# Optimization experiments

Hardware: AMD Instinct MI355X
Metric: run time of the kernel (lower is better)

The kernel has to match this reference:

```python
import jax, jax.numpy as jnp
import numpy as np

BITS = 4
GROUP = 128
M, K, N = 16, 4096, 11008


def setup_inputs() -> dict:
    key = jax.random.key(0)
    k1, k2, k3 = jax.random.split(key, 3)
    A = jax.random.normal(k1, (M, K), dtype=jnp.float16)
    # packed 4-bit weights: 2 nibbles per byte, stored as int32 holding 0..255
    qweight = jax.random.randint(k2, (N, K * BITS // 8), 0, 256, dtype=jnp.int32)
    # small positive-ish scales like real GPTQ checkpoints
    scales = (jax.random.normal(k3, (N, K // GROUP)) * 0.01 + 0.02).astype(jnp.float16)
    zeros = jnp.zeros((N, K // GROUP), dtype=jnp.float16)
    bias = jnp.zeros((N,), dtype=jnp.float16)
    return {"A": A, "qweight": qweight, "scales": scales, "zeros": zeros, "bias": bias}


def _dequant(qweight, scales, zeros):
    # qweight: (N, K//2) packed; element idx -> byte idx//2, low nibble if idx even
    low = qweight & 0xF
    high = (qweight >> 4) & 0xF
    w_int = jnp.stack([low, high], axis=-1).reshape(qweight.shape[0], -1)  # (N, K)
    # per-group dequant with 'original' zeros: W = (q - z) * s
    s = jnp.repeat(scales, GROUP, axis=1)  # (N, K)
    z = jnp.repeat(zeros, GROUP, axis=1)   # (N, K)
    return (w_int.astype(jnp.float16) - z) * s


def reference(A, qweight, scales, zeros, bias):
    W = _dequant(qweight, scales, zeros)           # (N, K) fp16
    return jnp.matmul(A, W.T) + bias               # (M, N) fp16
```

## Files before the change

kernel.cpp:

```cpp
#include <hip/hip_runtime.h>

#define KK 4096
#define NN 11008
#define NGRP 32
#define KW 2048
#define WS_RS_OFF 131072
#define WS_SZ_OFF 139264

using short8  = __attribute__((ext_vector_type(8))) short;
using float4v = __attribute__((ext_vector_type(4))) float;

static __device__ __forceinline__ unsigned int pack_bf16(float lo, float hi) {
    unsigned int ul = __builtin_bit_cast(unsigned int, lo);
    unsigned int uh = __builtin_bit_cast(unsigned int, hi);
    ul = (ul + 0x7FFFu + ((ul >> 16) & 1u)) >> 16;
    uh = (uh + 0x7FFFu + ((uh >> 16) & 1u)) & 0xFFFF0000u;
    return ul | uh;
}
static __device__ __forceinline__ float bf16val(float f) {
    unsigned int u = __builtin_bit_cast(unsigned int, f);
    u = (u + 0x7FFFu + ((u >> 16) & 1u)) & 0xFFFF0000u;
    return __builtin_bit_cast(float, u);
}

__global__ __launch_bounds__(256) void prep_kernel(
    const float* __restrict__ A, const float* __restrict__ scales,
    const float* __restrict__ zeros, unsigned short* __restrict__ wsA,
    float* __restrict__ rowsum, float* __restrict__ SZ)
{
    const int b = blockIdx.x, t = threadIdx.x;
    if (b < 32) {
        const int tid = b * 256 + t;
        const int c = tid >> 6, l = tid & 63;
        const float* src = A + (size_t)(l & 15) * KK + c * 32 + (l >> 4) * 8;
        float4v x0 = *(const float4v*)src;
        float4v x1 = *(const float4v*)(src + 4);
        union { short8 s8; unsigned int u[4]; } p;
        p.u[0] = pack_bf16(x0[0], x0[1]);
        p.u[1] = pack_bf16(x0[2], x0[3]);
        p.u[2] = pack_bf16(x1[0], x1[1]);
        p.u[3] = pack_bf16(x1[2], x1[3]);
        *(short8*)(wsA + (size_t)tid * 8) = p.s8;
    } else if (b < 64) {
        const int sid = (b - 32) * 16 + (t >> 4);
        const int m = sid >> 5, g = sid & 31, j = t & 15;
        const float* p = A + (size_t)m * KK + g * 128 + j * 8;
        float4v x0 = *(const float4v*)p;
        float4v x1 = *(const float4v*)(p + 4);
        float sum = bf16val(x0[0]) + bf16val(x0[1]) + bf16val(x0[2]) + bf16val(x0[3])
                  + bf16val(x1[0]) + bf16val(x1[1]) + bf16val(x1[2]) + bf16val(x1[3]);
        sum += __shfl_xor(sum, 1, 16);
        sum += __shfl_xor(sum, 2, 16);
        sum += __shfl_xor(sum, 4, 16);
        sum += __shfl_xor(sum, 8, 16);
        if (j == 0) rowsum[sid] = sum;
    } else {
        const int e0 = (b - 64) * 1024 + t * 4;
        float4v s4 = *(const float4v*)(scales + e0);
        float4v z4 = *(const float4v*)(zeros + e0);
        float4v r;
        #pragma unroll
        for (int j = 0; j < 4; ++j) r[j] = s4[j] * (128.0f + z4[j]);
        *(float4v*)(SZ + e0) = r;
    }
}

__global__ __launch_bounds__(256) void init_out_kernel(
    const float* __restrict__ bias, const float* __restrict__ SZ,
    const float* __restrict__ rowsum, float* __restrict__ out)
{
    __shared__ float rs[16][32];
    const int t = threadIdx.x;
    rs[t >> 5][t & 31]       = rowsum[t];
    rs[(t >> 5) + 8][t & 31] = rowsum[t + 256];
    __syncthreads();
    const int n0 = blockIdx.x * 16;
    const int m = t >> 4, nn = t & 15, ng = n0 + nn;
    const float* szr = SZ + (size_t)ng * NGRP;
    float corr = 0.f;
    #pragma unroll
    for (int g = 0; g < 32; ++g)
        corr = __builtin_fmaf(szr[g], rs[m][g], corr);
    out[(size_t)m * NN + ng] = bias[ng] - corr;
}

__global__ __launch_bounds__(256) void qgemm_kernel(
    const int*            __restrict__ qweight,
    const float*          __restrict__ scales,
    const unsigned short* __restrict__ aperm,
    float*                __restrict__ out)
{
    const int nt = blockIdx.x >> 3, slice = blockIdx.x & 7;
    const int n0 = nt * 16;
    const int wid = threadIdx.x >> 6, lane = threadIdx.x & 63;
    const int nl = lane & 15, quad = lane >> 4;
    const int n = n0 + nl;
    const int g = slice * 4 + wid;

    const int* qrow = qweight + (size_t)n * KW + g * 64 + quad * 4;
    const unsigned short* ap = aperm + (size_t)g * 2048 + lane * 8;

    int4   w0 = *(const int4*)(qrow);
    int4   w1 = *(const int4*)(qrow + 16);
    int4   w2 = *(const int4*)(qrow + 32);
    int4   w3 = *(const int4*)(qrow + 48);
    short8 a0 = *(const short8*)(ap);
    short8 a1 = *(const short8*)(ap + 512);
    short8 a2 = *(const short8*)(ap + 1024);
    short8 a3 = *(const short8*)(ap + 1536);
    const float s = scales[n * NGRP + g];

    float4v acc = {0.f, 0.f, 0.f, 0.f};
    int4 wv[4] = {w0, w1, w2, w3};
    short8 av[4] = {a0, a1, a2, a3};
    #pragma unroll
    for (int t = 0; t < 4; ++t) {
        const unsigned int x0 = (unsigned int)wv[t].x, x1 = (unsigned int)wv[t].y;
        const unsigned int x2 = (unsigned int)wv[t].z, x3 = (unsigned int)wv[t].w;
        union { short8 s8; unsigned int u[4]; } bf;
        bf.u[0] = (x0 & 0xFu) | ((x0 << 12) & 0x000F0000u) | 0x43004300u;
        bf.u[1] = (x1 & 0xFu) | ((x1 << 12) & 0x000F0000u) | 0x43004300u;
        bf.u[2] = (x2 & 0xFu) | ((x2 << 12) & 0x000F0000u) | 0x43004300u;
        bf.u[3] = (x3 & 0xFu) | ((x3 << 12) & 0x000F0000u) | 0x43004300u;
        acc = __builtin_amdgcn_mfma_f32_16x16x32_bf16(av[t], bf.s8, acc, 0, 0, 0);
    }

    __shared__ float red[4][16][16];
    #pragma unroll
    for (int r = 0; r < 4; ++r)
        red[wid][quad * 4 + r][nl] = s * acc[r];
    __syncthreads();

    const int t = threadIdx.x;
    const int m = t >> 4, nn = t & 15;
    float val = red[0][m][nn] + red[1][m][nn] + red[2][m][nn] + red[3][m][nn];
    atomicAdd(&out[(size_t)m * NN + n0 + nn], val);
}

extern "C" void kernel_launch(void* const* d_in, const int* in_sizes, int n_in,
                              void* d_out, int out_size, void* d_ws, size_t ws_size,
                              hipStream_t stream) {
    const float* A       = (const float*)d_in[0];
    const int*   qweight = (const int*)d_in[1];
    const float* scales  = (const float*)d_in[2];
    const float* zeros   = (const float*)d_in[3];
    const float* bias    = (const float*)d_in[4];
    float*       out     = (float*)d_out;

    unsigned short* wsA = (unsigned short*)d_ws;
    float* rowsum       = (float*)((char*)d_ws + WS_RS_OFF);
    float* SZ           = (float*)((char*)d_ws + WS_SZ_OFF);

    prep_kernel<<<dim3(408), dim3(256), 0, stream>>>(A, scales, zeros, wsA, rowsum, SZ);
    init_out_kernel<<<dim3(688), dim3(256), 0, stream>>>(bias, SZ, rowsum, out);
    qgemm_kernel<<<dim3(5504), dim3(256), 0, stream>>>(qweight, scales, wsA, out);
}
```

Measured before the change: 144.3 us.

## Stage weight tiles through LDS with coalesced loads and larger K-slices per block

Each block now covers half of K for 16 output columns instead of one eighth. It first loads a 64KB weight tile with fully coalesced row-contiguous 16-byte loads into shared memory, then each wave reads its MFMA operands from LDS and applies per-group scales in registers. This replaces strided per-lane global reads of qweight and cuts the number of blocks and atomics by a factor of four. In exchange, the large LDS footprint limits occupancy, and there is a serial load-then-compute phase with no overlap.

Result: slower. 148.1 us (+2.6%).

```diff
diff --git a/kernel.cpp b/kernel.cpp
--- a/kernel.cpp
+++ b/kernel.cpp
@@ -84,56 +84,71 @@
     out[(size_t)m * NN + ng] = bias[ng] - corr;
 }
 
-__global__ __launch_bounds__(256) void qgemm_kernel(
+__global__ __launch_bounds__(256, 2) void qgemm_kernel(
     const int*            __restrict__ qweight,
     const float*          __restrict__ scales,
     const unsigned short* __restrict__ aperm,
     float*                __restrict__ out)
 {
-    const int nt = blockIdx.x >> 3, slice = blockIdx.x & 7;
+    __shared__ __align__(16) char tile[65536];
+
+    const int nt = blockIdx.x >> 1, kh = blockIdx.x & 1;
     const int n0 = nt * 16;
     const int wid = threadIdx.x >> 6, lane = threadIdx.x & 63;
     const int nl = lane & 15, quad = lane >> 4;
-    const int n = n0 + nl;
-    const int g = slice * 4 + wid;
 
-    const int* qrow = qweight + (size_t)n * KW + g * 64 + quad * 4;
-    const unsigned short* ap = aperm + (size_t)g * 2048 + lane * 8;
+    const char* gbase = (const char*)qweight + (size_t)n0 * 8192 + kh * 4096;
+    int4 stg[16];
+    #pragma unroll
+    for (int i = 0; i < 16; ++i) {
+        const int r = wid * 4 + (i >> 2), c = i & 3;
+        stg[i] = *(const int4*)(gbase + (size_t)r * 8192 + c * 1024 + (lane << 4));
+    }
+    #pragma unroll
+    for (int i = 0; i < 16; ++i) {
+        const int r = wid * 4 + (i >> 2), c = i & 3;
+        *(int4*)(tile + r * 4096 + c * 1024 + (lane << 4)) = stg[i];
+    }
+    __syncthreads();
 
-    int4   w0 = *(const int4*)(qrow);
-    int4   w1 = *(const int4*)(qrow + 16);
-    int4   w2 = *(const int4*)(qrow + 32);
-    int4   w3 = *(const int4*)(qrow + 48);
-    short8 a0 = *(const short8*)(ap);
-    short8 a1 = *(const short8*)(ap + 512);
-    short8 a2 = *(const short8*)(ap + 1024);
-    short8 a3 = *(const short8*)(ap + 1536);
-    const float s = scales[n * NGRP + g];
-
+    const float* srow = scales + (size_t)(n0 + nl) * NGRP + kh * 16 + wid * 4;
     float4v acc = {0.f, 0.f, 0.f, 0.f};
-    int4 wv[4] = {w0, w1, w2, w3};
-    short8 av[4] = {a0, a1, a2, a3};
     #pragma unroll
-    for (int t = 0; t < 4; ++t) {
-        const unsigned int x0 = (unsigned int)wv[t].x, x1 = (unsigned int)wv[t].y;
-        const unsigned int x2 = (unsigned int)wv[t].z, x3 = (unsigned int)wv[t].w;
-        union { short8 s8; unsigned int u[4]; } bf;
-        bf.u[0] = (x0 & 0xFu) | ((x0 << 12) & 0x000F0000u) | 0x43004300u;
-        bf.u[1] = (x1 & 0xFu) | ((x1 << 12) & 0x000F0000u) | 0x43004300u;
-        bf.u[2] = (x2 & 0xFu) | ((x2 << 12) & 0x000F0000u) | 0x43004300u;
-        bf.u[3] = (x3 & 0xFu) | ((x3 << 12) & 0x000F0000u) | 0x43004300u;
-        acc = __builtin_amdgcn_mfma_f32_16x16x32_bf16(av[t], bf.s8, acc, 0, 0, 0);
+    for (int gl = 0; gl < 4; ++gl) {
+        const int ch0 = wid * 16 + gl * 4;
+        float4v accg = {0.f, 0.f, 0.f, 0.f};
+        #pragma unroll
+        for (int t = 0; t < 4; ++t) {
+            const unsigned short* ap =
+                aperm + (size_t)(kh * 64 + ch0 + t) * 512 + lane * 8;
+            short8 a = *(const short8*)ap;
+            int4 wv = *(const int4*)(tile + nl * 4096 + (ch0 + t) * 64 + quad * 16);
+            const unsigned int x0 = (unsigned int)wv.x, x1 = (unsigned int)wv.y;
+            const unsigned int x2 = (unsigned int)wv.z, x3 = (unsigned int)wv.w;
+            union { short8 s8; unsigned int u[4]; } bf;
+            bf.u[0] = (x0 & 0xFu) | ((x0 << 12) & 0x000F0000u) | 0x43004300u;
+            bf.u[1] = (x1 & 0xFu) | ((x1 << 12) & 0x000F0000u) | 0x43004300u;
+            bf.u[2] = (x2 & 0xFu) | ((x2 << 12) & 0x000F0000u) | 0x43004300u;
+            bf.u[3] = (x3 & 0xFu) | ((x3 << 12) & 0x000F0000u) | 0x43004300u;
+            accg = __builtin_amdgcn_mfma_f32_16x16x32_bf16(a, bf.s8, accg, 0, 0, 0);
+        }
+        const float sg = srow[gl];
+        #pragma unroll
+        for (int r = 0; r < 4; ++r)
+            acc[r] = __builtin_fmaf(sg, accg[r], acc[r]);
     }
 
-    __shared__ float red[4][16][16];
+    __syncthreads();
+    float* red = (float*)tile;
     #pragma unroll
     for (int r = 0; r < 4; ++r)
-        red[wid][quad * 4 + r][nl] = s * acc[r];
+        red[wid * 256 + (quad * 4 + r) * 16 + nl] = acc[r];
     __syncthreads();
 
     const int t = threadIdx.x;
     const int m = t >> 4, nn = t & 15;
-    float val = red[0][m][nn] + red[1][m][nn] + red[2][m][nn] + red[3][m][nn];
+    float val = red[m * 16 + nn] + red[256 + m * 16 + nn]
+              + red[512 + m * 16 + nn] + red[768 + m * 16 + nn];
     atomicAdd(&out[(size_t)m * NN + n0 + nn], val);
 }
 
@@ -153,5 +168,5 @@
 
     prep_kernel<<<dim3(408), dim3(256), 0, stream>>>(A, scales, zeros, wsA, rowsum, SZ);
     init_out_kernel<<<dim3(688), dim3(256), 0, stream>>>(bias, SZ, rowsum, out);
-    qgemm_kernel<<<dim3(5504), dim3(256), 0, stream>>>(qweight, scales, wsA, out);
+    qgemm_kernel<<<dim3(1376), dim3(256), 0, stream>>>(qweight, scales, wsA, out);
 }
```

## Compact int32-per-byte weights into a packed byte buffer before the GEMM

Applied to the files above, without the earlier changes.

Adds a compaction stage to the prep kernel that reads the int32 qweight array and writes one byte per element into a workspace buffer. The layout is permuted so each GEMM lane gets its 16 bytes with a single 16-byte load instead of four. The GEMM then reads a quarter of the weight bytes. The catch is that the compaction runs on every call and must itself read the full 4-byte-per-element array and write the packed copy, so total memory traffic per call goes up rather than down.

Measured after the change: 156.3 us. +8.3%, slower.

```diff
diff --git a/kernel.cpp b/kernel.cpp
--- a/kernel.cpp
+++ b/kernel.cpp
@@ -3,9 +3,9 @@
 #define KK 4096
 #define NN 11008
 #define NGRP 32
-#define KW 2048
-#define WS_RS_OFF 131072
-#define WS_SZ_OFF 139264
+#define WS_RS_OFF  131072
+#define WS_SZ_OFF  139264
+#define WS_PK_OFF  2097152
 
 using short8  = __attribute__((ext_vector_type(8))) short;
 using float4v = __attribute__((ext_vector_type(4))) float;
@@ -23,14 +23,31 @@
     return __builtin_bit_cast(float, u);
 }
 
-__global__ __launch_bounds__(256) void prep_kernel(
-    const float* __restrict__ A, const float* __restrict__ scales,
-    const float* __restrict__ zeros, unsigned short* __restrict__ wsA,
-    float* __restrict__ rowsum, float* __restrict__ SZ)
+__global__ __launch_bounds__(256) void compact_prep_kernel(
+    const float* __restrict__ A, const int* __restrict__ qweight,
+    const float* __restrict__ scales, const float* __restrict__ zeros,
+    unsigned short* __restrict__ wsA, float* __restrict__ rowsum,
+    float* __restrict__ SZ, unsigned char* __restrict__ packed)
 {
     const int b = blockIdx.x, t = threadIdx.x;
-    if (b < 32) {
-        const int tid = b * 256 + t;
+    if (b < 5504) {
+        const int r  = t >> 7;
+        const int g  = (t >> 2) & 31;
+        const int tt = t & 3;
+        const size_t n = (size_t)b * 2 + r;
+        const int4* src = (const int4*)(qweight + n * 2048 + g * 64 + tt * 16);
+        unsigned char* dst = packed + n * 2048 + g * 64 + tt * 4;
+        #pragma unroll
+        for (int q = 0; q < 4; ++q) {
+            int4 v = src[q];
+            unsigned int d = ((unsigned int)v.x & 0xFFu)
+                           | (((unsigned int)v.y & 0xFFu) << 8)
+                           | (((unsigned int)v.z & 0xFFu) << 16)
+                           | (((unsigned int)v.w & 0xFFu) << 24);
+            *(unsigned int*)(dst + q * 16) = d;
+        }
+    } else if (b < 5536) {
+        const int tid = (b - 5504) * 256 + t;
         const int c = tid >> 6, l = tid & 63;
         const float* src = A + (size_t)(l & 15) * KK + c * 32 + (l >> 4) * 8;
         float4v x0 = *(const float4v*)src;
@@ -41,8 +58,8 @@
         p.u[2] = pack_bf16(x1[0], x1[1]);
         p.u[3] = pack_bf16(x1[2], x1[3]);
         *(short8*)(wsA + (size_t)tid * 8) = p.s8;
-    } else if (b < 64) {
-        const int sid = (b - 32) * 16 + (t >> 4);
+    } else if (b < 5568) {
+        const int sid = (b - 5536) * 16 + (t >> 4);
         const int m = sid >> 5, g = sid & 31, j = t & 15;
         const float* p = A + (size_t)m * KK + g * 128 + j * 8;
         float4v x0 = *(const float4v*)p;
@@ -55,7 +72,7 @@
         sum += __shfl_xor(sum, 8, 16);
         if (j == 0) rowsum[sid] = sum;
     } else {
-        const int e0 = (b - 64) * 1024 + t * 4;
+        const int e0 = (b - 5568) * 1024 + t * 4;
         float4v s4 = *(const float4v*)(scales + e0);
         float4v z4 = *(const float4v*)(zeros + e0);
         float4v r;
@@ -85,7 +102,7 @@
 }
 
 __global__ __launch_bounds__(256) void qgemm_kernel(
-    const int*            __restrict__ qweight,
+    const unsigned char*  __restrict__ packed,
     const float*          __restrict__ scales,
     const unsigned short* __restrict__ aperm,
     float*                __restrict__ out)
@@ -97,13 +114,10 @@
     const int n = n0 + nl;
     const int g = slice * 4 + wid;
 
-    const int* qrow = qweight + (size_t)n * KW + g * 64 + quad * 4;
+    const int4* wp = (const int4*)(packed + (size_t)n * 2048 + g * 64 + quad * 16);
     const unsigned short* ap = aperm + (size_t)g * 2048 + lane * 8;
 
-    int4   w0 = *(const int4*)(qrow);
-    int4   w1 = *(const int4*)(qrow + 16);
-    int4   w2 = *(const int4*)(qrow + 32);
-    int4   w3 = *(const int4*)(qrow + 48);
+    int4   wv = *wp;
     short8 a0 = *(const short8*)(ap);
     short8 a1 = *(const short8*)(ap + 512);
     short8 a2 = *(const short8*)(ap + 1024);
@@ -111,17 +125,18 @@
     const float s = scales[n * NGRP + g];
 
     float4v acc = {0.f, 0.f, 0.f, 0.f};
-    int4 wv[4] = {w0, w1, w2, w3};
+    const unsigned int dv[4] = {(unsigned int)wv.x, (unsigned int)wv.y,
+                                (unsigned int)wv.z, (unsigned int)wv.w};
     short8 av[4] = {a0, a1, a2, a3};
     #pragma unroll
     for (int t = 0; t < 4; ++t) {
-        const unsigned int x0 = (unsigned int)wv[t].x, x1 = (unsigned int)wv[t].y;
-        const unsigned int x2 = (unsigned int)wv[t].z, x3 = (unsigned int)wv[t].w;
+        const unsigned int d = dv[t];
+        const unsigned int c0 = d, c1 = d >> 8, c2 = d >> 16, c3 = d >> 24;
         union { short8 s8; unsigned int u[4]; } bf;
-        bf.u[0] = (x0 & 0xFu) | ((x0 << 12) & 0x000F0000u) | 0x43004300u;
-        bf.u[1] = (x1 & 0xFu) | ((x1 << 12) & 0x000F0000u) | 0x43004300u;
-        bf.u[2] = (x2 & 0xFu) | ((x2 << 12) & 0x000F0000u) | 0x43004300u;
-        bf.u[3] = (x3 & 0xFu) | ((x3 << 12) & 0x000F0000u) | 0x43004300u;
+        bf.u[0] = (c0 & 0xFu) | ((c0 << 12) & 0x000F0000u) | 0x43004300u;
+        bf.u[1] = (c1 & 0xFu) | ((c1 << 12) & 0x000F0000u) | 0x43004300u;
+        bf.u[2] = (c2 & 0xFu) | ((c2 << 12) & 0x000F0000u) | 0x43004300u;
+        bf.u[3] = (c3 & 0xFu) | ((c3 << 12) & 0x000F0000u) | 0x43004300u;
         acc = __builtin_amdgcn_mfma_f32_16x16x32_bf16(av[t], bf.s8, acc, 0, 0, 0);
     }
 
@@ -147,11 +162,13 @@
     const float* bias    = (const float*)d_in[4];
     float*       out     = (float*)d_out;
 
-    unsigned short* wsA = (unsigned short*)d_ws;
-    float* rowsum       = (float*)((char*)d_ws + WS_RS_OFF);
-    float* SZ           = (float*)((char*)d_ws + WS_SZ_OFF);
+    unsigned short* wsA   = (unsigned short*)d_ws;
+    float* rowsum         = (float*)((char*)d_ws + WS_RS_OFF);
+    float* SZ             = (float*)((char*)d_ws + WS_SZ_OFF);
+    unsigned char* packed = (unsigned char*)d_ws + WS_PK_OFF;
 
-    prep_kernel<<<dim3(408), dim3(256), 0, stream>>>(A, scales, zeros, wsA, rowsum, SZ);
+    compact_prep_kernel<<<dim3(5912), dim3(256), 0, stream>>>(
+        A, qweight, scales, zeros, wsA, rowsum, SZ, packed);
     init_out_kernel<<<dim3(688), dim3(256), 0, stream>>>(bias, SZ, rowsum, out);
-    qgemm_kernel<<<dim3(5504), dim3(256), 0, stream>>>(qweight, scales, wsA, out);
+    qgemm_kernel<<<dim3(5504), dim3(256), 0, stream>>>(packed, scales, wsA, out);
 }
```

## Fold zero-point/bias correction into qgemm epilogue and drop init kernel

Applied to the files above, without the earlier changes.

Removes the separate init_out kernel and the scales×zeros precompute in prep. The first K-slice block of each N tile now computes bias minus the rowsum×scale×(128+zero) correction and adds it through its atomicAdd. Weight loads switch to nontemporal loads to avoid polluting the cache with streamed data. This saves one launch and the extra output/SZ traffic, at the cost of a 32-step correction loop in slice-0 blocks. It also now relies on the output buffer starting at zero, because out is no longer written before the atomic accumulation.

Result: slower. 182.2 us (+26.3%).

```diff
diff --git a/kernel.cpp b/kernel.cpp
--- a/kernel.cpp
+++ b/kernel.cpp
@@ -3,12 +3,11 @@
 #define KK 4096
 #define NN 11008
 #define NGRP 32
-#define KW 2048
 #define WS_RS_OFF 131072
-#define WS_SZ_OFF 139264
 
 using short8  = __attribute__((ext_vector_type(8))) short;
 using float4v = __attribute__((ext_vector_type(4))) float;
+using int4v   = __attribute__((ext_vector_type(4))) int;
 
 static __device__ __forceinline__ unsigned int pack_bf16(float lo, float hi) {
     unsigned int ul = __builtin_bit_cast(unsigned int, lo);
@@ -24,9 +23,8 @@
 }
 
 __global__ __launch_bounds__(256) void prep_kernel(
-    const float* __restrict__ A, const float* __restrict__ scales,
-    const float* __restrict__ zeros, unsigned short* __restrict__ wsA,
-    float* __restrict__ rowsum, float* __restrict__ SZ)
+    const float* __restrict__ A, unsigned short* __restrict__ wsA,
+    float* __restrict__ rowsum)
 {
     const int b = blockIdx.x, t = threadIdx.x;
     if (b < 32) {
@@ -41,7 +39,7 @@
         p.u[2] = pack_bf16(x1[0], x1[1]);
         p.u[3] = pack_bf16(x1[2], x1[3]);
         *(short8*)(wsA + (size_t)tid * 8) = p.s8;
-    } else if (b < 64) {
+    } else {
         const int sid = (b - 32) * 16 + (t >> 4);
         const int m = sid >> 5, g = sid & 31, j = t & 15;
         const float* p = A + (size_t)m * KK + g * 128 + j * 8;
@@ -54,40 +52,16 @@
         sum += __shfl_xor(sum, 4, 16);
         sum += __shfl_xor(sum, 8, 16);
         if (j == 0) rowsum[sid] = sum;
-    } else {
-        const int e0 = (b - 64) * 1024 + t * 4;
-        float4v s4 = *(const float4v*)(scales + e0);
-        float4v z4 = *(const float4v*)(zeros + e0);
-        float4v r;
-        #pragma unroll
-        for (int j = 0; j < 4; ++j) r[j] = s4[j] * (128.0f + z4[j]);
-        *(float4v*)(SZ + e0) = r;
     }
-}
-
-__global__ __launch_bounds__(256) void init_out_kernel(
-    const float* __restrict__ bias, const float* __restrict__ SZ,
-    const float* __restrict__ rowsum, float* __restrict__ out)
-{
-    __shared__ float rs[16][32];
-    const int t = threadIdx.x;
-    rs[t >> 5][t & 31]       = rowsum[t];
-    rs[(t >> 5) + 8][t & 31] = rowsum[t + 256];
-    __syncthreads();
-    const int n0 = blockIdx.x * 16;
-    const int m = t >> 4, nn = t & 15, ng = n0 + nn;
-    const float* szr = SZ + (size_t)ng * NGRP;
-    float corr = 0.f;
-    #pragma unroll
-    for (int g = 0; g < 32; ++g)
-        corr = __builtin_fmaf(szr[g], rs[m][g], corr);
-    out[(size_t)m * NN + ng] = bias[ng] - corr;
 }
 
 __global__ __launch_bounds__(256) void qgemm_kernel(
     const int*            __restrict__ qweight,
     const float*          __restrict__ scales,
+    const float*          __restrict__ zeros,
+    const float*          __restrict__ bias,
     const unsigned short* __restrict__ aperm,
+    const float*          __restrict__ rowsum,
     float*                __restrict__ out)
 {
     const int nt = blockIdx.x >> 3, slice = blockIdx.x & 7;
@@ -97,13 +71,13 @@
     const int n = n0 + nl;
     const int g = slice * 4 + wid;
 
-    const int* qrow = qweight + (size_t)n * KW + g * 64 + quad * 4;
+    const int4v* qp = (const int4v*)(qweight + (size_t)n * 2048 + g * 64 + quad * 4);
     const unsigned short* ap = aperm + (size_t)g * 2048 + lane * 8;
 
-    int4   w0 = *(const int4*)(qrow);
-    int4   w1 = *(const int4*)(qrow + 16);
-    int4   w2 = *(const int4*)(qrow + 32);
-    int4   w3 = *(const int4*)(qrow + 48);
+    int4v  w0 = __builtin_nontemporal_load(qp);
+    int4v  w1 = __builtin_nontemporal_load(qp + 4);
+    int4v  w2 = __builtin_nontemporal_load(qp + 8);
+    int4v  w3 = __builtin_nontemporal_load(qp + 12);
     short8 a0 = *(const short8*)(ap);
     short8 a1 = *(const short8*)(ap + 512);
     short8 a2 = *(const short8*)(ap + 1024);
@@ -111,12 +85,12 @@
     const float s = scales[n * NGRP + g];
 
     float4v acc = {0.f, 0.f, 0.f, 0.f};
-    int4 wv[4] = {w0, w1, w2, w3};
+    int4v  wv[4] = {w0, w1, w2, w3};
     short8 av[4] = {a0, a1, a2, a3};
     #pragma unroll
     for (int t = 0; t < 4; ++t) {
-        const unsigned int x0 = (unsigned int)wv[t].x, x1 = (unsigned int)wv[t].y;
-        const unsigned int x2 = (unsigned int)wv[t].z, x3 = (unsigned int)wv[t].w;
+        const unsigned int x0 = (unsigned int)wv[t][0], x1 = (unsigned int)wv[t][1];
+        const unsigned int x2 = (unsigned int)wv[t][2], x3 = (unsigned int)wv[t][3];
         union { short8 s8; unsigned int u[4]; } bf;
         bf.u[0] = (x0 & 0xFu) | ((x0 << 12) & 0x000F0000u) | 0x43004300u;
         bf.u[1] = (x1 & 0xFu) | ((x1 << 12) & 0x000F0000u) | 0x43004300u;
@@ -133,8 +107,20 @@
 
     const int t = threadIdx.x;
     const int m = t >> 4, nn = t & 15;
+    const int ng = n0 + nn;
     float val = red[0][m][nn] + red[1][m][nn] + red[2][m][nn] + red[3][m][nn];
-    atomicAdd(&out[(size_t)m * NN + n0 + nn], val);
+
+    if (slice == 0) {
+        const float* sr = scales + (size_t)ng * NGRP;
+        const float* zr = zeros  + (size_t)ng * NGRP;
+        const float* rs = rowsum + m * NGRP;
+        float corr = 0.f;
+        #pragma unroll
+        for (int gg = 0; gg < 32; ++gg)
+            corr = __builtin_fmaf(sr[gg] * (128.0f + zr[gg]), rs[gg], corr);
+        val += bias[ng] - corr;
+    }
+    atomicAdd(&out[(size_t)m * NN + ng], val);
 }
 
 extern "C" void kernel_launch(void* const* d_in, const int* in_sizes, int n_in,
@@ -149,9 +135,8 @@
 
     unsigned short* wsA = (unsigned short*)d_ws;
     float* rowsum       = (float*)((char*)d_ws + WS_RS_OFF);
-    float* SZ           = (float*)((char*)d_ws + WS_SZ_OFF);
 
-    prep_kernel<<<dim3(408), dim3(256), 0, stream>>>(A, scales, zeros, wsA, rowsum, SZ);
-    init_out_kernel<<<dim3(688), dim3(256), 0, stream>>>(bias, SZ, rowsum, out);
-    qgemm_kernel<<<dim3(5504), dim3(256), 0, stream>>>(qweight, scales, wsA, out);
+    prep_kernel<<<dim3(64), dim3(256), 0, stream>>>(A, wsA, rowsum);
+    qgemm_kernel<<<dim3(5504), dim3(256), 0, stream>>>(
+        qweight, scales, zeros, bias, wsA, rowsum, out);
 }
```
